# Kernel optimization log

Hardware: AMD Instinct MI355X
Metric: run time of the kernel (lower is better)

## Reference

```python
import jax, jax.numpy as jnp
import numpy as np

B, S, D, H, L = 32, 512, 1024, 1024, 2
SCALE = 1.0 / np.sqrt(H)  # keep activations sane


def setup_inputs() -> dict:
    key = jax.random.key(0)
    ks = jax.random.split(key, 9)
    return {
        "x":   jax.random.normal(ks[0], (B, S, D), dtype=jnp.float32),
        "Wx0": jax.random.normal(ks[1], (4 * H, D), dtype=jnp.float32) * SCALE,
        "Wh0": jax.random.normal(ks[2], (4 * H, H), dtype=jnp.float32) * SCALE,
        "bx0": jax.random.normal(ks[3], (4 * H,), dtype=jnp.float32) * SCALE,
        "bh0": jax.random.normal(ks[4], (4 * H,), dtype=jnp.float32) * SCALE,
        "Wx1": jax.random.normal(ks[5], (4 * H, H), dtype=jnp.float32) * SCALE,
        "Wh1": jax.random.normal(ks[6], (4 * H, H), dtype=jnp.float32) * SCALE,
        "bx1": jax.random.normal(ks[7], (4 * H,), dtype=jnp.float32) * SCALE,
        "bh1": jax.random.normal(ks[8], (4 * H,), dtype=jnp.float32) * SCALE,
    }


def reference(x, Wx0, Wh0, bx0, bh0, Wx1, Wh1, bx1, bh1):
    Wx, Wh, bx, bh = [Wx0, Wx1], [Wh0, Wh1], [bx0, bx1], [bh0, bh1]

    def step(carry, x_t):
        h, c = carry                      # each [L, B, H]
        inp = x_t                         # [B, D]
        hs, cs = [], []
        for l in range(L):
            gates = inp @ Wx[l].T + bx[l] + h[l] @ Wh[l].T + bh[l]  # [B, 4H]
            f, i, g, o = jnp.split(gates, 4, axis=1)  # torch chunk order: f,i,g,o
            c_new = jax.nn.sigmoid(f) * c[l] + jax.nn.sigmoid(i) * jnp.tanh(g)
            h_new = jax.nn.sigmoid(o) * jnp.tanh(c_new)  # proj is Identity
            hs.append(h_new)
            cs.append(c_new)
            inp = h_new  # dropout p=0 -> identity
        return (jnp.stack(hs), jnp.stack(cs)), hs[-1]

    h0 = jnp.zeros((L, B, H), dtype=x.dtype)
    c0 = jnp.zeros((L, B, H), dtype=x.dtype)
    (h_n, c_n), outs = jax.lax.scan(step, (h0, c0), jnp.transpose(x, (1, 0, 2)))
    outputs = jnp.transpose(outs, (1, 0, 2))  # [B, S, H] (batch_first)
    return outputs, (h_n, c_n)
```

## Files before the change

### kernel.cpp

```cpp
#include <hip/hip_runtime.h>
#include <math.h>

#define Bsz 32
#define Ssz 512
#define Hsz 1024

typedef _Float16 f16x8 __attribute__((ext_vector_type(8)));
typedef float    f32x4 __attribute__((ext_vector_type(4)));
typedef float    f32x8 __attribute__((ext_vector_type(8)));
typedef unsigned u32x4 __attribute__((ext_vector_type(4)));

struct P {
  const float *x, *Wx0, *Wh0, *bx0, *bh0, *Wx1, *Wh1, *bx1, *bh1;
  unsigned *h0r;
  unsigned *h1r;
  unsigned *f0, *f1;
  _Float16 *wsw;
  float *out;
};

__global__ __launch_bounds__(256) void preconv(P p) {
  unsigned idx   = blockIdx.x * 256 + threadIdx.x;
  unsigned lane  = idx & 63;
  unsigned m     = (idx >> 6) & 3;
  unsigned ks    = (idx >> 8) & 63;
  unsigned blk   = (idx >> 14) & 63;
  unsigned layer = idx >> 20;
  unsigned hidx  = blk * 16 + (lane & 15);
  unsigned k     = ks * 32 + (lane >> 4) * 8;
  unsigned row   = m * 1024 + hidx;
  const float* src;
  if (layer == 0) src = (k < 1024) ? p.Wx0 + (size_t)row * 1024 + k
                                   : p.Wh0 + (size_t)row * 1024 + (k - 1024);
  else            src = (k < 1024) ? p.Wx1 + (size_t)row * 1024 + k
                                   : p.Wh1 + (size_t)row * 1024 + (k - 1024);
  f32x8 v = *reinterpret_cast<const f32x8*>(src);
  f16x8 h;
#pragma unroll
  for (int j = 0; j < 8; ++j) h[j] = (_Float16)v[j];
  *reinterpret_cast<f16x8*>(p.wsw + (size_t)idx * 8) = h;
}

__device__ inline void load_xfrag(const float* xp, f16x8& Bh, f16x8& Bl) {
  f32x8 v = *reinterpret_cast<const f32x8*>(xp);
#pragma unroll
  for (int j = 0; j < 8; ++j) {
    _Float16 hv = (_Float16)v[j];
    Bh[j] = hv; Bl[j] = (_Float16)(v[j] - (float)hv);
  }
}

__global__ __launch_bounds__(512, 2) void lstm_persist(P p) {
  const int blk   = blockIdx.x;
  const int layer = blk >> 6;
  const int hb    = blk & 63;
  const int tid   = threadIdx.x;
  const int w     = tid >> 6;
  const int lane  = tid & 63;
  const int nl    = lane & 15;
  const int quad  = lane >> 4;

  __shared__ float red[8][64 * 33];
  __shared__ float csl[Bsz * 16];
  __shared__ float bsum[64];

  if (tid < 64) {
    int r = (tid >> 4) * 1024 + hb * 16 + (tid & 15);
    bsum[tid] = layer ? (p.bx1[r] + p.bh1[r]) : (p.bx0[r] + p.bh0[r]);
  }
  csl[tid] = 0.f;
  __syncthreads();

  const _Float16* wslab = p.wsw + (size_t)(layer * 64 + hb) * 131072;
  f16x8 Wr[32];
#pragma unroll
  for (int kk = 0; kk < 8; ++kk)
#pragma unroll
    for (int m = 0; m < 4; ++m)
      Wr[kk * 4 + m] = *reinterpret_cast<const f16x8*>(
          wslab + (size_t)(((w * 8 + kk) * 4 + m) * 64 + lane) * 8);

  const bool xwave = (layer == 0) && (w < 4);
  const int  kloc  = (w & 3) * 256;

  for (int s = 0; s < Ssz; ++s) {
    if (layer == 0) {
      if (xwave) {
        if (s >= 4) {
          const unsigned* fp = p.f1 + (s & 1) * 64 + lane;
          unsigned need = (unsigned)(s - 3);
          while (__hip_atomic_load(fp, __ATOMIC_RELAXED, __HIP_MEMORY_SCOPE_AGENT) < need) {}
        }
      } else if (s >= 1) {
        const unsigned* fp = p.f0 + ((s - 1) & 3) * 64 + (w & 3) * 16 + nl;
        unsigned need = (unsigned)s;
        while (__hip_atomic_load(fp, __ATOMIC_RELAXED, __HIP_MEMORY_SCOPE_AGENT) < need) {}
      }
    } else {
      if (w < 4) {
        const unsigned* fp = p.f0 + (s & 3) * 64 + (w & 3) * 16 + nl;
        unsigned need = (unsigned)(s + 1);
        while (__hip_atomic_load(fp, __ATOMIC_RELAXED, __HIP_MEMORY_SCOPE_AGENT) < need) {}
      } else if (s >= 1) {
        const unsigned* fp = p.f1 + ((s - 1) & 1) * 64 + (w & 3) * 16 + nl;
        unsigned need = (unsigned)s;
        while (__hip_atomic_load(fp, __ATOMIC_RELAXED, __HIP_MEMORY_SCOPE_AGENT) < need) {}
      }
    }

    f32x4 acc[4][2];
#pragma unroll
    for (int m = 0; m < 4; ++m)
#pragma unroll
      for (int nt = 0; nt < 2; ++nt) acc[m][nt] = (f32x4){0.f, 0.f, 0.f, 0.f};

    if (xwave) {
      const float* xbase = p.x + (size_t)s * 1024 + kloc;
      f16x8 Bh[2][2], Bl[2][2];
      load_xfrag(xbase + (size_t)nl        * (Ssz * 1024) + quad * 8, Bh[0][0], Bl[0][0]);
      load_xfrag(xbase + (size_t)(nl + 16) * (Ssz * 1024) + quad * 8, Bh[0][1], Bl[0][1]);
#pragma unroll
      for (int kk = 0; kk < 8; ++kk) {
        const int cur = kk & 1, nxt = cur ^ 1;
        if (kk < 7) {
          const int ko = (kk + 1) * 32 + quad * 8;
          load_xfrag(xbase + (size_t)nl        * (Ssz * 1024) + ko, Bh[nxt][0], Bl[nxt][0]);
          load_xfrag(xbase + (size_t)(nl + 16) * (Ssz * 1024) + ko, Bh[nxt][1], Bl[nxt][1]);
        }
#pragma unroll
        for (int m = 0; m < 4; ++m) {
          f16x8 A = Wr[kk * 4 + m];
#pragma unroll
          for (int nt = 0; nt < 2; ++nt) {
            acc[m][nt] = __builtin_amdgcn_mfma_f32_16x16x32_f16(A, Bh[cur][nt], acc[m][nt], 0, 0, 0);
            acc[m][nt] = __builtin_amdgcn_mfma_f32_16x16x32_f16(A, Bl[cur][nt], acc[m][nt], 0, 0, 0);
          }
        }
      }
    } else {
      const unsigned* bring;
      if (layer == 0) bring = p.h0r + ((s - 1) & 3) * 32768 + kloc;
      else if (w < 4) bring = p.h0r + (s & 3) * 32768 + kloc;
      else            bring = p.h1r + ((s - 1) & 1) * 32768 + kloc;
      const unsigned long long* q0 =
          (const unsigned long long*)(bring + nl * 1024) + quad * 4;
      const unsigned long long* q1 =
          (const unsigned long long*)(bring + (nl + 16) * 1024) + quad * 4;

      unsigned long long raw[3][8];
#define ISSUE(KK) do {                                                            \
      const unsigned long long* r0_ = q0 + (KK) * 16;                             \
      const unsigned long long* r1_ = q1 + (KK) * 16;                             \
      _Pragma("unroll")                                                           \
      for (int j_ = 0; j_ < 4; ++j_) {                                            \
        raw[(KK) % 3][j_]     = __hip_atomic_load(r0_ + j_, __ATOMIC_RELAXED,     \
                                                  __HIP_MEMORY_SCOPE_AGENT);      \
        raw[(KK) % 3][4 + j_] = __hip_atomic_load(r1_ + j_, __ATOMIC_RELAXED,     \
                                                  __HIP_MEMORY_SCOPE_AGENT);      \
      }                                                                           \
    } while (0)
#define UNPACK(BUF, OFF, BH, BL) do {                                             \
      u32x4 hw_, lw_;                                                             \
      _Pragma("unroll")                                                           \
      for (int j_ = 0; j_ < 4; ++j_) {                                            \
        unsigned long long u_ = raw[BUF][(OFF) + j_];                             \
        unsigned a_ = (unsigned)u_, b_ = (unsigned)(u_ >> 32);                    \
        hw_[j_] = (a_ & 0xffffu) | (b_ << 16);                                    \
        lw_[j_] = (a_ >> 16) | (b_ & 0xffff0000u);                                \
      }                                                                           \
      BH = __builtin_bit_cast(f16x8, hw_);                                        \
      BL = __builtin_bit_cast(f16x8, lw_);                                        \
    } while (0)

      ISSUE(0); ISSUE(1); ISSUE(2);
#pragma unroll
      for (int kk = 0; kk < 8; ++kk) {
        const int buf = kk % 3;
        f16x8 Bh0, Bl0, Bh1, Bl1;
        UNPACK(buf, 0, Bh0, Bl0);
        UNPACK(buf, 4, Bh1, Bl1);
        if (kk < 5) ISSUE(kk + 3);
#pragma unroll
        for (int m = 0; m < 4; ++m) {
          f16x8 A = Wr[kk * 4 + m];
          acc[m][0] = __builtin_amdgcn_mfma_f32_16x16x32_f16(A, Bh0, acc[m][0], 0, 0, 0);
          acc[m][0] = __builtin_amdgcn_mfma_f32_16x16x32_f16(A, Bl0, acc[m][0], 0, 0, 0);
          acc[m][1] = __builtin_amdgcn_mfma_f32_16x16x32_f16(A, Bh1, acc[m][1], 0, 0, 0);
          acc[m][1] = __builtin_amdgcn_mfma_f32_16x16x32_f16(A, Bl1, acc[m][1], 0, 0, 0);
        }
      }
#undef ISSUE
#undef UNPACK
    }

#pragma unroll
    for (int m = 0; m < 4; ++m)
#pragma unroll
      for (int nt = 0; nt < 2; ++nt)
#pragma unroll
        for (int r = 0; r < 4; ++r)
          red[w][(m * 16 + quad * 4 + r) * 33 + nt * 16 + nl] = acc[m][nt][r];
    __syncthreads();
#pragma unroll
    for (int j = 0; j < 4; ++j) {
      int idx = tid + j * 512;
      int ad = (idx >> 5) * 33 + (idx & 31);
      float ssum = red[0][ad] + red[1][ad] + red[2][ad] + red[3][ad]
                 + red[4][ad] + red[5][ad] + red[6][ad] + red[7][ad];
      red[0][ad] = ssum;
    }
    __syncthreads();

    {
      int hl = tid & 15, b = tid >> 4;
      float gf = red[0][(0 * 16 + hl) * 33 + b] + bsum[0 * 16 + hl];
      float gi = red[0][(1 * 16 + hl) * 33 + b] + bsum[1 * 16 + hl];
      float gg = red[0][(2 * 16 + hl) * 33 + b] + bsum[2 * 16 + hl];
      float go = red[0][(3 * 16 + hl) * 33 + b] + bsum[3 * 16 + hl];
      float f  = 1.f / (1.f + __expf(-gf));
      float i  = 1.f / (1.f + __expf(-gi));
      float g  = tanhf(gg);
      float o  = 1.f / (1.f + __expf(-go));
      float c  = f * csl[b * 16 + hl] + i * g;
      float hn = o * tanhf(c);
      csl[b * 16 + hl] = c;
      _Float16 hh  = (_Float16)hn;
      _Float16 hlo = (_Float16)(hn - (float)hh);
      unsigned pk = (unsigned)__builtin_bit_cast(unsigned short, hh)
                  | ((unsigned)__builtin_bit_cast(unsigned short, hlo) << 16);
      int hg = hb * 16 + hl;
      if (layer == 0) {
        __hip_atomic_store(p.h0r + (s & 3) * 32768 + b * 1024 + hg, pk,
                           __ATOMIC_RELAXED, __HIP_MEMORY_SCOPE_AGENT);
      } else {
        __hip_atomic_store(p.h1r + (s & 1) * 32768 + b * 1024 + hg, pk,
                           __ATOMIC_RELAXED, __HIP_MEMORY_SCOPE_AGENT);
        p.out[(size_t)b * (Ssz * Hsz) + (size_t)s * Hsz + hg] = hn;
      }
      if (s == Ssz - 1) {
        float* tail = p.out + (size_t)Bsz * Ssz * Hsz;
        tail[layer * 32768 + b * 1024 + hg] = hn;
        tail[65536 + layer * 32768 + b * 1024 + hg] = c;
      }
    }
    __syncthreads();
    if (tid == 0) {
      if (layer == 0)
        __hip_atomic_store(p.f0 + (s & 3) * 64 + hb, (unsigned)(s + 1),
                           __ATOMIC_RELAXED, __HIP_MEMORY_SCOPE_AGENT);
      else
        __hip_atomic_store(p.f1 + (s & 1) * 64 + hb, (unsigned)(s + 1),
                           __ATOMIC_RELAXED, __HIP_MEMORY_SCOPE_AGENT);
    }
  }
}

extern "C" void kernel_launch(void* const* d_in, const int* in_sizes, int n_in,
                              void* d_out, int out_size, void* d_ws, size_t ws_size,
                              hipStream_t stream) {
  char* ws = (char*)d_ws;
  P p;
  p.x   = (const float*)d_in[0];
  p.Wx0 = (const float*)d_in[1]; p.Wh0 = (const float*)d_in[2];
  p.bx0 = (const float*)d_in[3]; p.bh0 = (const float*)d_in[4];
  p.Wx1 = (const float*)d_in[5]; p.Wh1 = (const float*)d_in[6];
  p.bx1 = (const float*)d_in[7]; p.bh1 = (const float*)d_in[8];

  p.h0r = (unsigned*)(ws);
  p.h1r = (unsigned*)(ws + 524288);
  p.f0  = (unsigned*)(ws + 786432);
  p.f1  = (unsigned*)(ws + 788480);
  p.wsw = (_Float16*)(ws + 1048576);
  p.out = (float*)d_out;

  hipMemsetAsync(d_ws, 0, 1048576, stream);
  preconv<<<dim3(8192), dim3(256), 0, stream>>>(p);
  lstm_persist<<<dim3(128), dim3(512), 0, stream>>>(p);
}
```

Before: 8.924 ms.

## Store recurrent hidden state in MFMA fragment layout for direct vector loads

The producer now writes the hi and lo fp16 halves of h into a layout that matches the MFMA B-fragment, so consumers issue plain 16-byte vector loads after an acquire fence. This removes the per-element unpacking and the triple-buffered 64-bit atomic-load pipeline. In exchange the producer does two 16-bit atomic stores per element, which are scattered, and the explicit software prefetch is dropped, so consumers rely on the compiler to overlap loads with compute. Correctness depends on the acquire fence making the relaxed stores visible to the non-atomic loads.

Result: no change. 9.083 ms (+1.8%).

```diff
diff --git a/kernel.cpp b/kernel.cpp
--- a/kernel.cpp
+++ b/kernel.cpp
@@ -8,12 +8,11 @@
 typedef _Float16 f16x8 __attribute__((ext_vector_type(8)));
 typedef float    f32x4 __attribute__((ext_vector_type(4)));
 typedef float    f32x8 __attribute__((ext_vector_type(8)));
-typedef unsigned u32x4 __attribute__((ext_vector_type(4)));
 
 struct P {
   const float *x, *Wx0, *Wh0, *bx0, *bh0, *Wx1, *Wh1, *bx1, *bh1;
-  unsigned *h0r;
-  unsigned *h1r;
+  unsigned short *h0r;
+  unsigned short *h1r;
   unsigned *f0, *f1;
   _Float16 *wsw;
   float *out;
@@ -138,48 +137,19 @@
         }
       }
     } else {
-      const unsigned* bring;
-      if (layer == 0) bring = p.h0r + ((s - 1) & 3) * 32768 + kloc;
-      else if (w < 4) bring = p.h0r + (s & 3) * 32768 + kloc;
-      else            bring = p.h1r + ((s - 1) & 1) * 32768 + kloc;
-      const unsigned long long* q0 =
-          (const unsigned long long*)(bring + nl * 1024) + quad * 4;
-      const unsigned long long* q1 =
-          (const unsigned long long*)(bring + (nl + 16) * 1024) + quad * 4;
-
-      unsigned long long raw[3][8];
-#define ISSUE(KK) do {                                                            \
-      const unsigned long long* r0_ = q0 + (KK) * 16;                             \
-      const unsigned long long* r1_ = q1 + (KK) * 16;                             \
-      _Pragma("unroll")                                                           \
-      for (int j_ = 0; j_ < 4; ++j_) {                                            \
-        raw[(KK) % 3][j_]     = __hip_atomic_load(r0_ + j_, __ATOMIC_RELAXED,     \
-                                                  __HIP_MEMORY_SCOPE_AGENT);      \
-        raw[(KK) % 3][4 + j_] = __hip_atomic_load(r1_ + j_, __ATOMIC_RELAXED,     \
-                                                  __HIP_MEMORY_SCOPE_AGENT);      \
-      }                                                                           \
-    } while (0)
-#define UNPACK(BUF, OFF, BH, BL) do {                                             \
-      u32x4 hw_, lw_;                                                             \
-      _Pragma("unroll")                                                           \
-      for (int j_ = 0; j_ < 4; ++j_) {                                            \
-        unsigned long long u_ = raw[BUF][(OFF) + j_];                             \
-        unsigned a_ = (unsigned)u_, b_ = (unsigned)(u_ >> 32);                    \
-        hw_[j_] = (a_ & 0xffffu) | (b_ << 16);                                    \
-        lw_[j_] = (a_ >> 16) | (b_ & 0xffff0000u);                                \
-      }                                                                           \
-      BH = __builtin_bit_cast(f16x8, hw_);                                        \
-      BL = __builtin_bit_cast(f16x8, lw_);                                        \
-    } while (0)
-
-      ISSUE(0); ISSUE(1); ISSUE(2);
+      __builtin_amdgcn_fence(__ATOMIC_ACQUIRE, "agent");
+      const unsigned short* rbase;
+      if (layer == 0) rbase = p.h0r + ((s - 1) & 3) * 65536;
+      else if (w < 4) rbase = p.h0r + (s & 3) * 65536;
+      else            rbase = p.h1r + ((s - 1) & 1) * 65536;
+      const _Float16* fb = (const _Float16*)rbase + ((w & 3) * 32 + quad) * 512 + nl * 16;
 #pragma unroll
       for (int kk = 0; kk < 8; ++kk) {
-        const int buf = kk % 3;
-        f16x8 Bh0, Bl0, Bh1, Bl1;
-        UNPACK(buf, 0, Bh0, Bl0);
-        UNPACK(buf, 4, Bh1, Bl1);
-        if (kk < 5) ISSUE(kk + 3);
+        const _Float16* fp2 = fb + kk * 2048;
+        f16x8 Bh0 = *reinterpret_cast<const f16x8*>(fp2);
+        f16x8 Bl0 = *reinterpret_cast<const f16x8*>(fp2 + 8);
+        f16x8 Bh1 = *reinterpret_cast<const f16x8*>(fp2 + 256);
+        f16x8 Bl1 = *reinterpret_cast<const f16x8*>(fp2 + 264);
 #pragma unroll
         for (int m = 0; m < 4; ++m) {
           f16x8 A = Wr[kk * 4 + m];
@@ -189,8 +159,6 @@
           acc[m][1] = __builtin_amdgcn_mfma_f32_16x16x32_f16(A, Bl1, acc[m][1], 0, 0, 0);
         }
       }
-#undef ISSUE
-#undef UNPACK
     }
 
 #pragma unroll
@@ -226,15 +194,19 @@
       csl[b * 16 + hl] = c;
       _Float16 hh  = (_Float16)hn;
       _Float16 hlo = (_Float16)(hn - (float)hh);
-      unsigned pk = (unsigned)__builtin_bit_cast(unsigned short, hh)
-                  | ((unsigned)__builtin_bit_cast(unsigned short, hlo) << 16);
-      int hg = hb * 16 + hl;
+      unsigned short hbits = __builtin_bit_cast(unsigned short, hh);
+      unsigned short lbits = __builtin_bit_cast(unsigned short, hlo);
+      int hg   = hb * 16 + hl;
+      int koct = hb * 2 + (hl >> 3), jj = hl & 7;
+      int fragoff = koct * 512 + b * 16 + jj;
       if (layer == 0) {
-        __hip_atomic_store(p.h0r + (s & 3) * 32768 + b * 1024 + hg, pk,
-                           __ATOMIC_RELAXED, __HIP_MEMORY_SCOPE_AGENT);
+        unsigned short* dst = p.h0r + (s & 3) * 65536 + fragoff;
+        __hip_atomic_store(dst,     hbits, __ATOMIC_RELAXED, __HIP_MEMORY_SCOPE_AGENT);
+        __hip_atomic_store(dst + 8, lbits, __ATOMIC_RELAXED, __HIP_MEMORY_SCOPE_AGENT);
       } else {
-        __hip_atomic_store(p.h1r + (s & 1) * 32768 + b * 1024 + hg, pk,
-                           __ATOMIC_RELAXED, __HIP_MEMORY_SCOPE_AGENT);
+        unsigned short* dst = p.h1r + (s & 1) * 65536 + fragoff;
+        __hip_atomic_store(dst,     hbits, __ATOMIC_RELAXED, __HIP_MEMORY_SCOPE_AGENT);
+        __hip_atomic_store(dst + 8, lbits, __ATOMIC_RELAXED, __HIP_MEMORY_SCOPE_AGENT);
         p.out[(size_t)b * (Ssz * Hsz) + (size_t)s * Hsz + hg] = hn;
       }
       if (s == Ssz - 1) {
@@ -266,8 +238,8 @@
   p.Wx1 = (const float*)d_in[5]; p.Wh1 = (const float*)d_in[6];
   p.bx1 = (const float*)d_in[7]; p.bh1 = (const float*)d_in[8];
 
-  p.h0r = (unsigned*)(ws);
-  p.h1r = (unsigned*)(ws + 524288);
+  p.h0r = (unsigned short*)(ws);
+  p.h1r = (unsigned short*)(ws + 524288);
   p.f0  = (unsigned*)(ws + 786432);
   p.f1  = (unsigned*)(ws + 788480);
   p.wsw = (_Float16*)(ws + 1048576);
```
